# Kernel tuning notes

Measured on AMD Instinct MI355X. Metric: run time of the kernel, lower is better.

The kernel has to match this reference:

```python
import jax, jax.numpy as jnp
import numpy as np

EPS = 1e-08


def setup_inputs() -> dict:
    key = jax.random.key(0)
    k1, k2 = jax.random.split(key)
    B, N = 64, 1024
    lower = jax.random.normal(k1, (B, N), dtype=jnp.float32)
    # upper >= lower; gap ~ U[0,2) so we get active (l>=0), inactive (u<=0), and crossing neurons
    upper = lower + 2.0 * jax.random.uniform(k2, (B, N), dtype=jnp.float32)
    return {"lower": lower, "upper": upper}


def reference(lower, upper):
    # Concrete interval bounds through ReLU
    concrete_lower = jnp.maximum(lower, 0.0)
    concrete_upper = jnp.maximum(upper, 0.0)

    active = lower >= 0                      # [B, N] identity relaxation
    crossing = (lower < 0) & (upper > 0)     # [B, N] linear upper relaxation

    lambda_upper = jnp.where(crossing, upper / (upper - lower + EPS), 0.0)  # [B, N]
    mu_upper = jnp.where(crossing, -lambda_upper * lower, 0.0)              # [B, N]

    # Per-neuron diagonal coefficients (only the diagonal is ever nonzero)
    lower_diag = active.astype(lower.dtype)                       # 1 if active else 0
    upper_diag = jnp.where(active, jnp.ones_like(lambda_upper), lambda_upper)

    n = lower.shape[1]
    eye = jnp.eye(n, dtype=lower.dtype)                           # [N, N]
    lower_coef = eye * lower_diag[:, :, None]                     # [B, N, N] dense diagonal
    upper_coef = eye * upper_diag[:, :, None]                     # [B, N, N] dense diagonal

    lower_bias = jnp.zeros_like(lower)
    upper_bias = mu_upper

    return (concrete_lower, concrete_upper, lower_coef, upper_coef, lower_bias, upper_bias)
```

## Files before the change

### kernel.cpp

```cpp
#include <hip/hip_runtime.h>

#define EPS 1e-8f

typedef float f32x4 __attribute__((ext_vector_type(4)));


__global__ void __launch_bounds__(256)
fused_kernel(const float* __restrict__ lower,
             const float* __restrict__ upper,
             float* __restrict__ out) {
    const int lane = threadIdx.x & 63;
    const int W = blockIdx.x * 4 + (threadIdx.x >> 6);
    const int start = W * 16 + (W < 256 ? W : 256);
    const int count = (W < 256) ? 17 : 16;

    for (int ri = 0; ri < count; ++ri) {
        const int vr = start + ri;
        if (vr < 131072) {
            const int rr = vr & 65535;
            const float l = lower[rr];
            const float u = upper[rr];
            const bool active = (l >= 0.0f);
            const bool crossing = (l < 0.0f) && (u > 0.0f);
            const float lam = crossing ? u / (u - l + EPS) : 0.0f;
            const float v = active ? 1.0f : (vr < 65536 ? 0.0f : lam);
            const int i = vr & 1023;
            f32x4* rp = (f32x4*)(out + 131072 + (size_t)vr * 1024) + lane;
            const int base = lane * 4;
#pragma unroll
            for (int k = 0; k < 4; ++k) {
                const int b = base + k * 256;
                f32x4 z;
                z.x = (b + 0 == i) ? v : 0.0f;
                z.y = (b + 1 == i) ? v : 0.0f;
                z.z = (b + 2 == i) ? v : 0.0f;
                z.w = (b + 3 == i) ? v : 0.0f;
                rp[k * 64] = z;
            }
        } else if (vr < 131136) {
            f32x4* rp = (f32x4*)(out + 134348800LL +
                                 (size_t)(vr - 131072) * 1024) + lane;
            const f32x4 z = {0.0f, 0.0f, 0.0f, 0.0f};
#pragma unroll
            for (int k = 0; k < 4; ++k) rp[k * 64] = z;
        } else if (vr < 131200) {
            const int r = vr - 131136;
            const f32x4* lp = (const f32x4*)(lower + (size_t)r * 1024) + lane;
            f32x4* rp = (f32x4*)(out + (size_t)r * 1024) + lane;
#pragma unroll
            for (int k = 0; k < 4; ++k) {
                f32x4 a = lp[k * 64];
                a.x = fmaxf(a.x, 0.0f);
                a.y = fmaxf(a.y, 0.0f);
                a.z = fmaxf(a.z, 0.0f);
                a.w = fmaxf(a.w, 0.0f);
                rp[k * 64] = a;
            }
        } else if (vr < 131264) {
            const int r = vr - 131200;
            const f32x4* up = (const f32x4*)(upper + (size_t)r * 1024) + lane;
            f32x4* rp = (f32x4*)(out + 65536 + (size_t)r * 1024) + lane;
#pragma unroll
            for (int k = 0; k < 4; ++k) {
                f32x4 a = up[k * 64];
                a.x = fmaxf(a.x, 0.0f);
                a.y = fmaxf(a.y, 0.0f);
                a.z = fmaxf(a.z, 0.0f);
                a.w = fmaxf(a.w, 0.0f);
                rp[k * 64] = a;
            }
        } else {
            const int r = vr - 131264;
            const f32x4* lp = (const f32x4*)(lower + (size_t)r * 1024) + lane;
            const f32x4* up = (const f32x4*)(upper + (size_t)r * 1024) + lane;
            f32x4* rp = (f32x4*)(out + 134414336LL + (size_t)r * 1024) + lane;
#pragma unroll
            for (int k = 0; k < 4; ++k) {
                f32x4 lv = lp[k * 64];
                f32x4 uv = up[k * 64];
                f32x4 m;
#pragma unroll
                for (int e = 0; e < 4; ++e) {
                    float l = lv[e], u = uv[e];
                    bool crossing = (l < 0.0f) && (u > 0.0f);
                    float lam = crossing ? u / (u - l + EPS) : 0.0f;
                    m[e] = crossing ? -lam * l : 0.0f;
                }
                rp[k * 64] = m;
            }
        }
    }
}

extern "C" void kernel_launch(void* const* d_in, const int* in_sizes, int n_in,
                              void* d_out, int out_size, void* d_ws, size_t ws_size,
                              hipStream_t stream) {
    const float* lower = (const float*)d_in[0];
    const float* upper = (const float*)d_in[1];
    float* out = (float*)d_out;

    fused_kernel<<<2048, 256, 0, stream>>>(lower, upper, out);
}
```

Baseline: 122.3 us.

## Assign one 1024-float row per block and launch one block per CU

Work is re-partitioned so that each 256-thread block writes a whole 1024-float row at a time, with each thread storing one float4, instead of each wavefront writing a row in four float4 strides. The grid shrinks from 2048 blocks to 256 persistent blocks of 513 rows each, and launch_bounds is set to one block per CU. The aim is to cut per-row index and branch overhead and to make the stores streaming-friendly. The trade-off is far fewer waves in flight (4 per CU), which may leave write bandwidth underused on a store-bound kernel.

Measured after the change: 180.4 us. 1.47x slower.

```diff
diff --git a/kernel.cpp b/kernel.cpp
--- a/kernel.cpp
+++ b/kernel.cpp
@@ -5,89 +5,68 @@
 typedef float f32x4 __attribute__((ext_vector_type(4)));
 
 
-__global__ void __launch_bounds__(256)
-fused_kernel(const float* __restrict__ lower,
-             const float* __restrict__ upper,
-             float* __restrict__ out) {
-    const int lane = threadIdx.x & 63;
-    const int W = blockIdx.x * 4 + (threadIdx.x >> 6);
-    const int start = W * 16 + (W < 256 ? W : 256);
-    const int count = (W < 256) ? 17 : 16;
+__global__ void __launch_bounds__(256, 1)
+fused_fill_kernel(const float* __restrict__ lower,
+                  const float* __restrict__ upper,
+                  float* __restrict__ out) {
+    const int tid = threadIdx.x;
+    const long long vr0 = (long long)blockIdx.x * 513;
 
-    for (int ri = 0; ri < count; ++ri) {
-        const int vr = start + ri;
-        if (vr < 131072) {
-            const int rr = vr & 65535;
-            const float l = lower[rr];
-            const float u = upper[rr];
-            const bool active = (l >= 0.0f);
-            const bool crossing = (l < 0.0f) && (u > 0.0f);
-            const float lam = crossing ? u / (u - l + EPS) : 0.0f;
-            const float v = active ? 1.0f : (vr < 65536 ? 0.0f : lam);
-            const int i = vr & 1023;
-            f32x4* rp = (f32x4*)(out + 131072 + (size_t)vr * 1024) + lane;
-            const int base = lane * 4;
-#pragma unroll
-            for (int k = 0; k < 4; ++k) {
-                const int b = base + k * 256;
-                f32x4 z;
-                z.x = (b + 0 == i) ? v : 0.0f;
-                z.y = (b + 1 == i) ? v : 0.0f;
-                z.z = (b + 2 == i) ? v : 0.0f;
-                z.w = (b + 3 == i) ? v : 0.0f;
-                rp[k * 64] = z;
-            }
-        } else if (vr < 131136) {
-            f32x4* rp = (f32x4*)(out + 134348800LL +
-                                 (size_t)(vr - 131072) * 1024) + lane;
+    int ncoef = (int)(131072 - vr0);
+    if (ncoef > 513) ncoef = 513;
+    float* dst = out + 131072 + vr0 * 1024 + tid * 4;
+#pragma unroll 4
+    for (int ri = 0; ri < ncoef; ++ri) {
+        const int vr = (int)vr0 + ri;
+        const int rr = vr & 65535;
+        const float l = lower[rr];
+        const float u = upper[rr];
+        const bool active = (l >= 0.0f);
+        const bool crossing = (l < 0.0f) && (u > 0.0f);
+        const float lam = crossing ? u / (u - l + EPS) : 0.0f;
+        const float v = active ? 1.0f : (vr < 65536 ? 0.0f : lam);
+        const int i = vr & 1023;
+        f32x4 z = {0.0f, 0.0f, 0.0f, 0.0f};
+        if ((i >> 2) == tid) z[i & 3] = v;
+        *(f32x4*)dst = z;
+        dst += 1024;
+    }
+
+    for (int ri = ncoef; ri < 513; ++ri) {
+        const int vr = (int)vr0 + ri;
+        if (vr < 131136) {
+            const int r = vr - 131072;
             const f32x4 z = {0.0f, 0.0f, 0.0f, 0.0f};
-#pragma unroll
-            for (int k = 0; k < 4; ++k) rp[k * 64] = z;
+            *((f32x4*)(out + 134348800LL + (long long)r * 1024) + tid) = z;
         } else if (vr < 131200) {
             const int r = vr - 131136;
-            const f32x4* lp = (const f32x4*)(lower + (size_t)r * 1024) + lane;
-            f32x4* rp = (f32x4*)(out + (size_t)r * 1024) + lane;
-#pragma unroll
-            for (int k = 0; k < 4; ++k) {
-                f32x4 a = lp[k * 64];
-                a.x = fmaxf(a.x, 0.0f);
-                a.y = fmaxf(a.y, 0.0f);
-                a.z = fmaxf(a.z, 0.0f);
-                a.w = fmaxf(a.w, 0.0f);
-                rp[k * 64] = a;
-            }
+            f32x4 a = *((const f32x4*)(lower + (size_t)r * 1024) + tid);
+            a.x = fmaxf(a.x, 0.0f);
+            a.y = fmaxf(a.y, 0.0f);
+            a.z = fmaxf(a.z, 0.0f);
+            a.w = fmaxf(a.w, 0.0f);
+            *((f32x4*)(out + (size_t)r * 1024) + tid) = a;
         } else if (vr < 131264) {
             const int r = vr - 131200;
-            const f32x4* up = (const f32x4*)(upper + (size_t)r * 1024) + lane;
-            f32x4* rp = (f32x4*)(out + 65536 + (size_t)r * 1024) + lane;
-#pragma unroll
-            for (int k = 0; k < 4; ++k) {
-                f32x4 a = up[k * 64];
-                a.x = fmaxf(a.x, 0.0f);
-                a.y = fmaxf(a.y, 0.0f);
-                a.z = fmaxf(a.z, 0.0f);
-                a.w = fmaxf(a.w, 0.0f);
-                rp[k * 64] = a;
-            }
+            f32x4 a = *((const f32x4*)(upper + (size_t)r * 1024) + tid);
+            a.x = fmaxf(a.x, 0.0f);
+            a.y = fmaxf(a.y, 0.0f);
+            a.z = fmaxf(a.z, 0.0f);
+            a.w = fmaxf(a.w, 0.0f);
+            *((f32x4*)(out + 65536 + (size_t)r * 1024) + tid) = a;
         } else {
             const int r = vr - 131264;
-            const f32x4* lp = (const f32x4*)(lower + (size_t)r * 1024) + lane;
-            const f32x4* up = (const f32x4*)(upper + (size_t)r * 1024) + lane;
-            f32x4* rp = (f32x4*)(out + 134414336LL + (size_t)r * 1024) + lane;
+            f32x4 lv = *((const f32x4*)(lower + (size_t)r * 1024) + tid);
+            f32x4 uv = *((const f32x4*)(upper + (size_t)r * 1024) + tid);
+            f32x4 m;
 #pragma unroll
-            for (int k = 0; k < 4; ++k) {
-                f32x4 lv = lp[k * 64];
-                f32x4 uv = up[k * 64];
-                f32x4 m;
-#pragma unroll
-                for (int e = 0; e < 4; ++e) {
-                    float l = lv[e], u = uv[e];
-                    bool crossing = (l < 0.0f) && (u > 0.0f);
-                    float lam = crossing ? u / (u - l + EPS) : 0.0f;
-                    m[e] = crossing ? -lam * l : 0.0f;
-                }
-                rp[k * 64] = m;
+            for (int e = 0; e < 4; ++e) {
+                float l = lv[e], u = uv[e];
+                bool crossing = (l < 0.0f) && (u > 0.0f);
+                float lam = crossing ? u / (u - l + EPS) : 0.0f;
+                m[e] = crossing ? -lam * l : 0.0f;
             }
+            *((f32x4*)(out + 134414336LL + (size_t)r * 1024) + tid) = m;
         }
     }
 }
@@ -99,5 +78,5 @@
     const float* upper = (const float*)d_in[1];
     float* out = (float*)d_out;
 
-    fused_kernel<<<2048, 256, 0, stream>>>(lower, upper, out);
+    fused_fill_kernel<<<256, 256, 0, stream>>>(lower, upper, out);
 }
```
